# Performance work log

Measured on AMD Instinct MI355X. Metric: run time of the kernel, lower is better.

## Reference

```python
import jax, jax.numpy as jnp
import numpy as np

H = 16      # num_head
D = 1024    # feat_dim
DK = D // H # per-head dim
B, S = 2, 2048


def setup_inputs() -> dict:
    key = jax.random.key(0)
    ks = jax.random.split(key, 11)
    scale = 1.0 / np.sqrt(D)
    inp = {
        'query': jax.random.normal(ks[0], (B, S, D), jnp.float32),
        'key':   jax.random.normal(ks[1], (B, S, D), jnp.float32),
        'value': jax.random.normal(ks[2], (B, S, D), jnp.float32),
        # causal lower-triangular mask (seq, seq); 0 entries get -1e9
        'mask':  jnp.tril(jnp.ones((S, S), jnp.int32)),
        # torch nn.Linear params: y = x @ W.T + b
        'w_q': jax.random.normal(ks[3], (D, D), jnp.float32) * scale,
        'b_q': jax.random.normal(ks[4], (D,), jnp.float32) * scale,
        'w_k': jax.random.normal(ks[5], (D, D), jnp.float32) * scale,
        'b_k': jax.random.normal(ks[6], (D,), jnp.float32) * scale,
        'w_v': jax.random.normal(ks[7], (D, D), jnp.float32) * scale,
        'b_v': jax.random.normal(ks[8], (D,), jnp.float32) * scale,
        'w_out': jax.random.normal(ks[9], (D, D), jnp.float32) * scale,
        'b_out': jax.random.normal(ks[10], (D,), jnp.float32) * scale,
    }
    return inp


def reference(query, key, value, mask, w_q, b_q, w_k, b_k, w_v, b_v, w_out, b_out):
    b = query.shape[0]
    # projections + split heads -> (b, h, s, d_k)
    def proj(x, w, bias):
        y = x @ w.T + bias
        return y.reshape(b, -1, H, DK).transpose(0, 2, 1, 3)
    q = proj(query, w_q, b_q)
    k = proj(key, w_k, b_k)
    v = proj(value, w_v, b_v)
    # scaled dot-product attention with materialized score matrix
    scores = jnp.einsum('bhqd,bhkd->bhqk', q, k) / np.sqrt(DK).astype(jnp.float32)
    scores = jnp.where(mask == 0, jnp.float32(-1e9), scores)
    attn = jax.nn.softmax(scores, axis=-1)  # dropout is identity in eval mode
    x = jnp.einsum('bhqk,bhkd->bhqd', attn, v)
    x = x.transpose(0, 2, 1, 3).reshape(b, -1, H * DK)
    return x @ w_out.T + b_out
```

## Files before the change

### kernel.cpp

```cpp
#include <hip/hip_runtime.h>

typedef unsigned short u16;
typedef __attribute__((ext_vector_type(8))) short short8;
typedef __attribute__((ext_vector_type(8))) unsigned short u16x8;
typedef __attribute__((ext_vector_type(4))) float floatx4;
typedef __attribute__((ext_vector_type(16))) float floatx16;

#define S2LOG 0.18033688f

__device__ __forceinline__ u16 f2bf(float f) {
    unsigned int u = __float_as_uint(f);
    return (u16)((u + 0x7FFFu + ((u >> 16) & 1u)) >> 16);
}
__device__ __forceinline__ void gl_lds16(const u16* g, u16* l) {
    __builtin_amdgcn_global_load_lds(
        (const __attribute__((address_space(1))) void*)g,
        (__attribute__((address_space(3))) void*)l, 16, 0, 0);
}

__global__ __launch_bounds__(256) void cvt_all(
    const float* __restrict__ q, const float* __restrict__ k, const float* __restrict__ v,
    const float* __restrict__ wq, const float* __restrict__ wk,
    const float* __restrict__ wv, const float* __restrict__ wo,
    u16* __restrict__ ws)
{
    const int b = blockIdx.x, t = threadIdx.x;
    const float* src; u16* dst; long blk;
    if      (b < 2048) { src = q;  dst = ws;            blk = b; }
    else if (b < 4096) { src = k;  dst = ws + 4194304;  blk = b - 2048; }
    else if (b < 6144) { src = v;  dst = ws + 8388608;  blk = b - 4096; }
    else if (b < 6656) { src = wq; dst = ws + 12582912; blk = b - 6144; }
    else if (b < 7168) { src = wk; dst = ws + 13631488; blk = b - 6656; }
    else if (b < 7680) { src = wv; dst = ws + 14680064; blk = b - 7168; }
    else               { src = wo; dst = ws + 15728640; blk = b - 7680; }
    const long i = blk * 2048 + (long)t * 8;
    const float4 a = *(const float4*)(src + i);
    const float4 c = *(const float4*)(src + i + 4);
    u16x8 o;
    o[0] = f2bf(a.x); o[1] = f2bf(a.y); o[2] = f2bf(a.z); o[3] = f2bf(a.w);
    o[4] = f2bf(c.x); o[5] = f2bf(c.y); o[6] = f2bf(c.z); o[7] = f2bf(c.w);
    *(u16x8*)(dst + i) = o;
}

__device__ __forceinline__ void gemm_core64(
    const u16* __restrict__ A, const u16* __restrict__ Bw,
    int m0, int n0, floatx4 (&acc)[2][4])
{
    __shared__ u16 As[2][128 * 64];
    __shared__ u16 Bs[2][64 * 64];
    const int t = threadIdx.x, w = t >> 6;
    const int lane = t & 63, col = lane & 15, quad = lane >> 4;
    const int c7 = col & 7;

#pragma unroll
    for (int i = 0; i < 2; ++i)
#pragma unroll
        for (int j = 0; j < 4; ++j) acc[i][j] = (floatx4)0.f;

    auto stage = [&](int k0, int buf) {
#pragma unroll
        for (int jj = 0; jj < 4; ++jj) {
            const int c = jj * 256 + t;
            const int row = c >> 3, kc = (c & 7) ^ (row & 7);
            gl_lds16(A + (size_t)(m0 + row) * 1024 + k0 + kc * 8,
                     As[buf] + (jj * 256 + w * 64) * 8);
        }
#pragma unroll
        for (int jj = 0; jj < 2; ++jj) {
            const int c = jj * 256 + t;
            const int row = c >> 3, kc = (c & 7) ^ (row & 7);
            gl_lds16(Bw + (size_t)(n0 + row) * 1024 + k0 + kc * 8,
                     Bs[buf] + (jj * 256 + w * 64) * 8);
        }
    };

    stage(0, 0);
    int cur = 0;
    for (int k0 = 0; k0 < 1024; k0 += 64) {
        asm volatile("s_waitcnt vmcnt(0)" ::: "memory");
        __builtin_amdgcn_s_barrier();
        if (k0 + 64 < 1024) stage(k0 + 64, cur ^ 1);
#pragma unroll
        for (int ks = 0; ks < 2; ++ks) {
            const int swz = (ks * 4 + quad) ^ c7;
            short8 af[2], bf[4];
#pragma unroll
            for (int i = 0; i < 2; ++i)
                af[i] = *(const short8*)&As[cur][((w * 32 + i * 16 + col) * 8 + swz) * 8];
#pragma unroll
            for (int j = 0; j < 4; ++j)
                bf[j] = *(const short8*)&Bs[cur][((j * 16 + col) * 8 + swz) * 8];
#pragma unroll
            for (int i = 0; i < 2; ++i)
#pragma unroll
                for (int j = 0; j < 4; ++j)
                    acc[i][j] = __builtin_amdgcn_mfma_f32_16x16x32_bf16(
                        af[i], bf[j], acc[i][j], 0, 0, 0);
        }
        asm volatile("s_waitcnt lgkmcnt(0)" ::: "memory");
        cur ^= 1;
    }
}

__device__ __forceinline__ void gemm_core128(
    const u16* __restrict__ A, const u16* __restrict__ Bw,
    int m0, int n0, floatx4 (&acc)[4][4])
{
    __shared__ u16 As[2][128 * 32];
    __shared__ u16 Bs[2][128 * 32];
    const int t = threadIdx.x, w = t >> 6;
    const int lane = t & 63, col = lane & 15, quad = lane >> 4;
    const int wr = (w >> 1) * 64, wc = (w & 1) * 64;
    const int swz = quad ^ (col & 3) ^ ((col >> 2) & 3);

#pragma unroll
    for (int i = 0; i < 4; ++i)
#pragma unroll
        for (int j = 0; j < 4; ++j) acc[i][j] = (floatx4)0.f;

    auto stage = [&](int k0, int buf) {
#pragma unroll
        for (int jj = 0; jj < 2; ++jj) {
            const int c = jj * 256 + t;
            const int row = c >> 2;
            const int kc = (c & 3) ^ (row & 3) ^ ((row >> 2) & 3);
            gl_lds16(A + (size_t)(m0 + row) * 1024 + k0 + kc * 8,
                     As[buf] + (jj * 256 + w * 64) * 8);
            gl_lds16(Bw + (size_t)(n0 + row) * 1024 + k0 + kc * 8,
                     Bs[buf] + (jj * 256 + w * 64) * 8);
        }
    };

    stage(0, 0);
    int cur = 0;
    for (int k0 = 0; k0 < 1024; k0 += 32) {
        asm volatile("s_waitcnt vmcnt(0)" ::: "memory");
        __builtin_amdgcn_s_barrier();
        if (k0 + 32 < 1024) stage(k0 + 32, cur ^ 1);
        short8 af[4], bf[4];
#pragma unroll
        for (int i = 0; i < 4; ++i)
            af[i] = *(const short8*)&As[cur][((wr + i * 16 + col) * 4 + swz) * 8];
#pragma unroll
        for (int j = 0; j < 4; ++j)
            bf[j] = *(const short8*)&Bs[cur][((wc + j * 16 + col) * 4 + swz) * 8];
        __builtin_amdgcn_s_setprio(1);
#pragma unroll
        for (int i = 0; i < 4; ++i)
#pragma unroll
            for (int j = 0; j < 4; ++j)
                acc[i][j] = __builtin_amdgcn_mfma_f32_16x16x32_bf16(
                    af[i], bf[j], acc[i][j], 0, 0, 0);
        __builtin_amdgcn_s_setprio(0);
        asm volatile("s_waitcnt lgkmcnt(0)" ::: "memory");
        cur ^= 1;
    }
}

__global__ __launch_bounds__(256) void gemm_qkv(
    const u16* __restrict__ xq, const u16* __restrict__ xk, const u16* __restrict__ xv,
    const u16* __restrict__ wqb, const u16* __restrict__ wkb, const u16* __restrict__ wvb,
    const float* __restrict__ bq, const float* __restrict__ bk, const float* __restrict__ bv,
    u16* __restrict__ Qh, u16* __restrict__ Kh, u16* __restrict__ Vt)
{
    const int z = blockIdx.z;
    const u16*   A    = z == 0 ? xq  : z == 1 ? xk  : xv;
    const u16*   Bw   = z == 0 ? wqb : z == 1 ? wkb : wvb;
    const float* bias = z == 0 ? bq  : z == 1 ? bk  : bv;
    u16*         out  = z == 0 ? Qh  : z == 1 ? Kh  : Vt;
    const float  scale = z == 0 ? S2LOG : 1.0f;
    const int m0 = blockIdx.x * 128, n0 = blockIdx.y * 128;

    floatx4 acc[4][4];
    gemm_core128(A, Bw, m0, n0, acc);

    const int t = threadIdx.x, w = t >> 6;
    const int lane = t & 63, col = lane & 15, quad = lane >> 4;
    const int wr = (w >> 1) * 64, wc = (w & 1) * 64;
#pragma unroll
    for (int i = 0; i < 4; ++i)
#pragma unroll
        for (int j = 0; j < 4; ++j)
#pragma unroll
            for (int reg = 0; reg < 4; ++reg) {
                const int gm = m0 + wr + i * 16 + quad * 4 + reg;
                const int gn = n0 + wc + j * 16 + col;
                const float val = (acc[i][j][reg] + bias[gn]) * scale;
                const int bb = gm >> 11, ss = gm & 2047, hh = gn >> 6, dd = gn & 63;
                if (z != 2)
                    out[(((size_t)bb * 16 + hh) * 2048 + ss) * 64 + dd] = f2bf(val);
                else
                    out[(((size_t)bb * 16 + hh) * 64 + dd) * 2048 + ss] = f2bf(val);
            }
}

__global__ __launch_bounds__(256) void gemm_out(
    const u16* __restrict__ A, const u16* __restrict__ Bw,
    const float* __restrict__ bias, float* __restrict__ out)
{
    const int m0 = blockIdx.x * 128, n0 = blockIdx.y * 64;
    floatx4 acc[2][4];
    gemm_core64(A, Bw, m0, n0, acc);
    const int t = threadIdx.x, w = t >> 6;
    const int lane = t & 63, col = lane & 15, quad = lane >> 4;
#pragma unroll
    for (int i = 0; i < 2; ++i)
#pragma unroll
        for (int j = 0; j < 4; ++j)
#pragma unroll
            for (int reg = 0; reg < 4; ++reg) {
                const int gm = m0 + w * 32 + i * 16 + quad * 4 + reg;
                const int gn = n0 + j * 16 + col;
                out[(size_t)gm * 1024 + gn] = acc[i][j][reg] + bias[gn];
            }
}

__global__ __launch_bounds__(256) void attn_mfma(
    const u16* __restrict__ Qh, const u16* __restrict__ Kh,
    const u16* __restrict__ Vt, u16* __restrict__ ctx)
{
    __shared__ u16 Qs[16 * 512];
    __shared__ u16 Ks[2][8 * 512];
    __shared__ u16 Vs[2][8 * 512];
    const int t = threadIdx.x, w = t >> 6;
    const int lane = t & 63;
    const int col = lane & 31;
    const int hi  = lane >> 5;
    const int bh = blockIdx.y;
    const int qt = (bh < 16) ? (15 - (int)blockIdx.x) : (int)blockIdx.x;
    const int q0 = qt * 128;
    const u16* qg = Qh + ((size_t)bh * 2048 + q0) * 64;
    const u16* kg = Kh + (size_t)bh * 2048 * 64;
    const u16* vg = Vt + (size_t)bh * 2048 * 64;

    auto stage = [&](int tile, int buf) {
#pragma unroll
        for (int jj = 0; jj < 2; ++jj) {
            const int cidx = jj * 4 + w;
            gl_lds16(kg + (size_t)(tile * 64 + jj * 32 + col) * 64 + w * 16 + hi * 8,
                     Ks[buf] + cidx * 512);
            gl_lds16(vg + (size_t)(jj * 32 + col) * 2048 + tile * 64 + w * 16 + hi * 8,
                     Vs[buf] + cidx * 512);
        }
    };

#pragma unroll
    for (int jj = 0; jj < 4; ++jj) {
        const int cidx = jj * 4 + w;
        gl_lds16(qg + (size_t)(jj * 32 + col) * 64 + w * 16 + hi * 8,
                 Qs + cidx * 512);
    }
    stage(0, 0);
    asm volatile("s_waitcnt vmcnt(4)" ::: "memory");
    __builtin_amdgcn_s_barrier();

    short8 qf[4];
#pragma unroll
    for (int tq = 0; tq < 4; ++tq)
        qf[tq] = *(const short8*)&Qs[(w * 4 + tq) * 512 + lane * 8];

    floatx16 oacc[2];
    oacc[0] = (floatx16)0.f; oacc[1] = (floatx16)0.f;
    float ls = 0.f;
    const int qrow = q0 + w * 32 + col;

    const int ktmax = 2 * qt + 1;
    int cur = 0;
    for (int kt = 0; kt <= ktmax; ++kt) {
        asm volatile("s_waitcnt vmcnt(0)" ::: "memory");
        __builtin_amdgcn_s_barrier();
        if (kt + 1 <= ktmax) stage(kt + 1, cur ^ 1);
        const bool pm = (kt >= 2 * qt);

#pragma unroll
        for (int sub = 0; sub < 2; ++sub) {
            short8 kf[4];
#pragma unroll
            for (int tq = 0; tq < 4; ++tq)
                kf[tq] = *(const short8*)&Ks[cur][(sub * 4 + tq) * 512 + lane * 8];

            floatx16 sacc = (floatx16)0.f;
#pragma unroll
            for (int tq = 0; tq < 4; ++tq)
                sacc = __builtin_amdgcn_mfma_f32_32x32x16_bf16(
                    kf[tq], qf[tq], sacc, 0, 0, 0);

            float pe[16];
#pragma unroll
            for (int r = 0; r < 16; ++r)
                pe[r] = __builtin_amdgcn_exp2f(sacc[r]);
            if (pm) {
                const int kbase = kt * 64 + sub * 32;
#pragma unroll
                for (int r = 0; r < 16; ++r) {
                    const int rkv = (r & 3) + 8 * (r >> 2) + 4 * hi;
                    if (kbase + rkv > qrow) pe[r] = 0.f;
                }
            }
#pragma unroll
            for (int r = 0; r < 16; ++r) ls += pe[r];

            short8 pa[2];
#pragma unroll
            for (int s = 0; s < 2; ++s) {
                unsigned A0, A1, B0, B1;
                asm("v_cvt_pk_bf16_f32 %0, %1, %2" : "=v"(A0) : "v"(pe[8*s+0]), "v"(pe[8*s+1]));
                asm("v_cvt_pk_bf16_f32 %0, %1, %2" : "=v"(A1) : "v"(pe[8*s+2]), "v"(pe[8*s+3]));
                asm("v_cvt_pk_bf16_f32 %0, %1, %2" : "=v"(B0) : "v"(pe[8*s+4]), "v"(pe[8*s+5]));
                asm("v_cvt_pk_bf16_f32 %0, %1, %2" : "=v"(B1) : "v"(pe[8*s+6]), "v"(pe[8*s+7]));
                asm("v_permlane32_swap_b32 %0, %1" : "+v"(A0), "+v"(B0));
                asm("v_permlane32_swap_b32 %0, %1" : "+v"(A1), "+v"(B1));
                union { unsigned u[4]; short8 s8; } cv;
                cv.u[0] = A0; cv.u[1] = A1; cv.u[2] = B0; cv.u[3] = B1;
                pa[s] = cv.s8;
            }

#pragma unroll
            for (int dt = 0; dt < 2; ++dt)
#pragma unroll
                for (int s = 0; s < 2; ++s) {
                    short8 vf = *(const short8*)
                        &Vs[cur][(dt * 4 + sub * 2 + s) * 512 + lane * 8];
                    oacc[dt] = __builtin_amdgcn_mfma_f32_32x32x16_bf16(
                        pa[s], vf, oacc[dt], 0, 0, 0);
                }
        }
        cur ^= 1;
    }

    const float lt = ls + __shfl_xor(ls, 32);
    const int bb = bh >> 4, hh = bh & 15;
#pragma unroll
    for (int reg = 0; reg < 16; ++reg) {
        const int qr = (reg & 3) + 8 * (reg >> 2) + 4 * hi;
        const float lq = __shfl(lt, qr, 64);
        const float inv = __builtin_amdgcn_rcpf(lq);
        const int qrs = q0 + w * 32 + qr;
#pragma unroll
        for (int dt = 0; dt < 2; ++dt)
            ctx[((size_t)bb * 2048 + qrs) * 1024 + hh * 64 + dt * 32 + col] =
                f2bf(oacc[dt][reg] * inv);
    }
}

extern "C" void kernel_launch(void* const* d_in, const int* in_sizes, int n_in,
                              void* d_out, int out_size, void* d_ws, size_t ws_size,
                              hipStream_t stream)
{
    const float* query = (const float*)d_in[0];
    const float* key   = (const float*)d_in[1];
    const float* value = (const float*)d_in[2];
    const float* w_q   = (const float*)d_in[4];
    const float* b_q   = (const float*)d_in[5];
    const float* w_k   = (const float*)d_in[6];
    const float* b_k   = (const float*)d_in[7];
    const float* w_v   = (const float*)d_in[8];
    const float* b_v   = (const float*)d_in[9];
    const float* w_out = (const float*)d_in[10];
    const float* b_out = (const float*)d_in[11];

    u16* W = (u16*)d_ws;
    u16* xq  = W;
    u16* xk  = W + 4194304;
    u16* xv  = W + 8388608;
    u16* wqb = W + 12582912;
    u16* wkb = W + 13631488;
    u16* wvb = W + 14680064;
    u16* wob = W + 15728640;
    u16* Qh  = W + 16777216;
    u16* Kh  = W + 20971520;
    u16* Vtw = W + 25165824;
    u16* ctx = W + 29360128;

    hipLaunchKernelGGL(cvt_all, dim3(8192), dim3(256), 0, stream,
                       query, key, value, w_q, w_k, w_v, w_out, W);

    hipLaunchKernelGGL(gemm_qkv, dim3(32, 8, 3), dim3(256), 0, stream,
                       xq, xk, xv, wqb, wkb, wvb, b_q, b_k, b_v, Qh, Kh, Vtw);

    hipLaunchKernelGGL(attn_mfma, dim3(16, 32), dim3(256), 0, stream, Qh, Kh, Vtw, ctx);

    hipLaunchKernelGGL(gemm_out, dim3(32, 16), dim3(256), 0, stream,
                       ctx, wob, b_out, (float*)d_out);
}
```

Before: 234.6 us.

## Split attention KV loop across two wave groups with LDS reduction

Doubles the attention block to 512 threads. Two groups of four waves take alternating key tiles for the same 128 query rows, each with its own double-buffered K/V in LDS. At the end, group 1 writes its partial output accumulators and row sums to LDS, and group 0 adds them, normalizes and stores. This is meant to halve the serial KV loop per block and raise wave-level parallelism, at the cost of more LDS per block, an extra reduction phase and possibly lower block occupancy.

After: 216.5 us. 1.08x faster.

```diff
diff --git a/kernel.cpp b/kernel.cpp
--- a/kernel.cpp
+++ b/kernel.cpp
@@ -215,14 +215,13 @@
             }
 }
 
-__global__ __launch_bounds__(256) void attn_mfma(
+__global__ __launch_bounds__(512) void attn_mfma(
     const u16* __restrict__ Qh, const u16* __restrict__ Kh,
     const u16* __restrict__ Vt, u16* __restrict__ ctx)
 {
-    __shared__ u16 Qs[16 * 512];
-    __shared__ u16 Ks[2][8 * 512];
-    __shared__ u16 Vs[2][8 * 512];
+    __shared__ u16 lds[40960];
     const int t = threadIdx.x, w = t >> 6;
+    const int g = w >> 2, wg = w & 3;
     const int lane = t & 63;
     const int col = lane & 31;
     const int hi  = lane >> 5;
@@ -233,51 +232,55 @@
     const u16* kg = Kh + (size_t)bh * 2048 * 64;
     const u16* vg = Vt + (size_t)bh * 2048 * 64;
 
+    u16* Qs = lds;
+    u16* Kg = lds + 8192 + g * 16384;
+    u16* Vg = Kg + 8192;
+
     auto stage = [&](int tile, int buf) {
 #pragma unroll
         for (int jj = 0; jj < 2; ++jj) {
-            const int cidx = jj * 4 + w;
-            gl_lds16(kg + (size_t)(tile * 64 + jj * 32 + col) * 64 + w * 16 + hi * 8,
-                     Ks[buf] + cidx * 512);
-            gl_lds16(vg + (size_t)(jj * 32 + col) * 2048 + tile * 64 + w * 16 + hi * 8,
-                     Vs[buf] + cidx * 512);
+            const int cidx = jj * 4 + wg;
+            gl_lds16(kg + (size_t)(tile * 64 + jj * 32 + col) * 64 + wg * 16 + hi * 8,
+                     Kg + buf * 4096 + cidx * 512);
+            gl_lds16(vg + (size_t)(jj * 32 + col) * 2048 + tile * 64 + wg * 16 + hi * 8,
+                     Vg + buf * 4096 + cidx * 512);
         }
     };
 
 #pragma unroll
-    for (int jj = 0; jj < 4; ++jj) {
-        const int cidx = jj * 4 + w;
-        gl_lds16(qg + (size_t)(jj * 32 + col) * 64 + w * 16 + hi * 8,
+    for (int jj = 0; jj < 2; ++jj) {
+        const int cidx = jj * 8 + w;
+        gl_lds16(qg + (size_t)((cidx >> 2) * 32 + col) * 64 + (cidx & 3) * 16 + hi * 8,
                  Qs + cidx * 512);
     }
-    stage(0, 0);
+    stage(g, 0);
     asm volatile("s_waitcnt vmcnt(4)" ::: "memory");
     __builtin_amdgcn_s_barrier();
 
     short8 qf[4];
 #pragma unroll
     for (int tq = 0; tq < 4; ++tq)
-        qf[tq] = *(const short8*)&Qs[(w * 4 + tq) * 512 + lane * 8];
+        qf[tq] = *(const short8*)&Qs[(wg * 4 + tq) * 512 + lane * 8];
 
     floatx16 oacc[2];
     oacc[0] = (floatx16)0.f; oacc[1] = (floatx16)0.f;
     float ls = 0.f;
-    const int qrow = q0 + w * 32 + col;
-
-    const int ktmax = 2 * qt + 1;
+    const int qrow = q0 + wg * 32 + col;
+
     int cur = 0;
-    for (int kt = 0; kt <= ktmax; ++kt) {
+    for (int i = 0; i <= qt; ++i) {
+        const int kt = 2 * i + g;
         asm volatile("s_waitcnt vmcnt(0)" ::: "memory");
         __builtin_amdgcn_s_barrier();
-        if (kt + 1 <= ktmax) stage(kt + 1, cur ^ 1);
-        const bool pm = (kt >= 2 * qt);
+        if (i + 1 <= qt) stage(2 * (i + 1) + g, cur ^ 1);
+        const bool pm = (i == qt);
 
 #pragma unroll
         for (int sub = 0; sub < 2; ++sub) {
             short8 kf[4];
 #pragma unroll
             for (int tq = 0; tq < 4; ++tq)
-                kf[tq] = *(const short8*)&Ks[cur][(sub * 4 + tq) * 512 + lane * 8];
+                kf[tq] = *(const short8*)&Kg[cur * 4096 + (sub * 4 + tq) * 512 + lane * 8];
 
             floatx16 sacc = (floatx16)0.f;
 #pragma unroll
@@ -320,7 +323,7 @@
 #pragma unroll
                 for (int s = 0; s < 2; ++s) {
                     short8 vf = *(const short8*)
-                        &Vs[cur][(dt * 4 + sub * 2 + s) * 512 + lane * 8];
+                        &Vg[cur * 4096 + (dt * 4 + sub * 2 + s) * 512 + lane * 8];
                     oacc[dt] = __builtin_amdgcn_mfma_f32_32x32x16_bf16(
                         pa[s], vf, oacc[dt], 0, 0, 0);
                 }
@@ -328,18 +331,43 @@
         cur ^= 1;
     }
 
-    const float lt = ls + __shfl_xor(ls, 32);
-    const int bb = bh >> 4, hh = bh & 15;
-#pragma unroll
-    for (int reg = 0; reg < 16; ++reg) {
-        const int qr = (reg & 3) + 8 * (reg >> 2) + 4 * hi;
-        const float lq = __shfl(lt, qr, 64);
-        const float inv = __builtin_amdgcn_rcpf(lq);
-        const int qrs = q0 + w * 32 + qr;
-#pragma unroll
-        for (int dt = 0; dt < 2; ++dt)
-            ctx[((size_t)bb * 2048 + qrs) * 1024 + hh * 64 + dt * 32 + col] =
-                f2bf(oacc[dt][reg] * inv);
+    asm volatile("s_waitcnt lgkmcnt(0)" ::: "memory");
+    __builtin_amdgcn_s_barrier();
+
+    float* Ob = (float*)(lds + 24576);
+    float* Lb = (float*)lds;
+    const int slot = wg * 64 + lane;
+    if (g == 1) {
+#pragma unroll
+        for (int r = 0; r < 16; ++r) {
+            Ob[slot * 32 + ((r + lane) & 31)]        = oacc[0][r];
+            Ob[slot * 32 + ((16 + r + lane) & 31)]   = oacc[1][r];
+        }
+        Lb[slot] = ls;
+    }
+    asm volatile("s_waitcnt lgkmcnt(0)" ::: "memory");
+    __builtin_amdgcn_s_barrier();
+    if (g == 0) {
+#pragma unroll
+        for (int r = 0; r < 16; ++r) {
+            oacc[0][r] += Ob[slot * 32 + ((r + lane) & 31)];
+            oacc[1][r] += Ob[slot * 32 + ((16 + r + lane) & 31)];
+        }
+        ls += Lb[slot];
+
+        const float lt = ls + __shfl_xor(ls, 32);
+        const int bb = bh >> 4, hh = bh & 15;
+#pragma unroll
+        for (int reg = 0; reg < 16; ++reg) {
+            const int qr = (reg & 3) + 8 * (reg >> 2) + 4 * hi;
+            const float lq = __shfl(lt, qr, 64);
+            const float inv = __builtin_amdgcn_rcpf(lq);
+            const int qrs = q0 + wg * 32 + qr;
+#pragma unroll
+            for (int dt = 0; dt < 2; ++dt)
+                ctx[((size_t)bb * 2048 + qrs) * 1024 + hh * 64 + dt * 32 + col] =
+                    f2bf(oacc[dt][reg] * inv);
+        }
     }
 }
 
@@ -378,7 +406,7 @@
     hipLaunchKernelGGL(gemm_qkv, dim3(32, 8, 3), dim3(256), 0, stream,
                        xq, xk, xv, wqb, wkb, wvb, b_q, b_k, b_v, Qh, Kh, Vtw);
 
-    hipLaunchKernelGGL(attn_mfma, dim3(16, 32), dim3(256), 0, stream, Qh, Kh, Vtw, ctx);
+    hipLaunchKernelGGL(attn_mfma, dim3(16, 32), dim3(512), 0, stream, Qh, Kh, Vtw, ctx);
 
     hipLaunchKernelGGL(gemm_out, dim3(32, 16), dim3(256), 0, stream,
                        ctx, wob, b_out, (float*)d_out);
```
